# Optimization experiments

Hardware: AMD Instinct MI355X
Metric: run time of the kernel (lower is better)

Reference implementation:

```python
import jax, jax.numpy as jnp
import numpy as np

D_MODEL = 1024
N_HEAD = 16
HEAD_DIM = D_MODEL // N_HEAD


def setup_inputs() -> dict:
    key = jax.random.key(0)
    ks = jax.random.split(key, 9)
    B, S, D = 2, 2048, D_MODEL
    s = 1.0 / np.sqrt(D)
    return {
        "x": jax.random.normal(ks[0], (B, S, D), dtype=jnp.float32),
        "Wq": jax.random.normal(ks[1], (D, D), dtype=jnp.float32) * s,
        "bq": jnp.zeros((D,), dtype=jnp.float32),
        "Wk": jax.random.normal(ks[2], (D, D), dtype=jnp.float32) * s,
        "bk": jnp.zeros((D,), dtype=jnp.float32),
        "Wv": jax.random.normal(ks[3], (D, D), dtype=jnp.float32) * s,
        "bv": jnp.zeros((D,), dtype=jnp.float32),
        "Wo": jax.random.normal(ks[4], (D, D), dtype=jnp.float32) * s,
        "bo": jnp.zeros((D,), dtype=jnp.float32),
    }


def _split_heads(t):
    B, S, D = t.shape
    return t.reshape(B, S, N_HEAD, HEAD_DIM).transpose(0, 2, 1, 3)  # [B,H,S,d]


def reference(x, Wq, bq, Wk, bk, Wv, bv, Wo, bo):
    B, S, D = x.shape
    q = _split_heads(x @ Wq + bq)
    k = _split_heads(x @ Wk + bk)
    v = _split_heads(x @ Wv + bv)
    present = jnp.stack((k, v))  # [2,B,H,S,d]
    # NOTE: module scales by sqrt(d_model), not sqrt(head_dim)
    scores = jnp.einsum("bhqd,bhkd->bhqk", q, k) / jnp.sqrt(jnp.float32(D_MODEL))
    causal = jnp.tril(jnp.ones((S, S), dtype=bool))
    scores = jnp.where(causal, scores, -jnp.inf)
    probs = jax.nn.softmax(scores, axis=-1)
    attn = jnp.einsum("bhqk,bhkd->bhqd", probs, v)
    attn = attn.transpose(0, 2, 1, 3).reshape(B, S, D)
    out = attn @ Wo + bo
    return out, present
```

## Files before the change

### kernel.cpp

```cpp
#include <hip/hip_runtime.h>
#include <hip/hip_bf16.h>

typedef __attribute__((ext_vector_type(8))) short short8;
typedef __attribute__((ext_vector_type(4))) short short4v;
typedef __attribute__((ext_vector_type(4))) float f32x4;

#define S_LEN 2048
#define DM 1024
#define NH 16
#define HD 64

__device__ __forceinline__ short f2b(float f) {
    __hip_bfloat16 h = __float2bfloat16(f);
    return *reinterpret_cast<short*>(&h);
}

__global__ void k_convert_x(const float* __restrict__ x, short* __restrict__ Af) {
    int t = blockIdx.x * 256 + threadIdx.x;
    int s = t >> 7, kc = t & 127;
    const float* xp = x + (size_t)s * DM + kc * 8;
    f32x4 v0 = *reinterpret_cast<const f32x4*>(xp);
    f32x4 v1 = *reinterpret_cast<const f32x4*>(xp + 4);
    short8 o;
    for (int e = 0; e < 4; e++) { o[e] = f2b(v0[e]); o[4 + e] = f2b(v1[e]); }
    int R = s >> 6, m = (s >> 4) & 3, lr = s & 15;
    int kstep = kc >> 3, ks = (kc >> 2) & 1, lg = kc & 3;
    size_t off = ((((size_t)(R * 16 + kstep) * 2 + ks) * 4 + m) * 64 + lg * 16 + lr) * 8;
    *reinterpret_cast<short8*>(Af + off) = o;
}

__global__ void k_transpose_w4(const float* __restrict__ W0, const float* __restrict__ W1,
                               const float* __restrict__ W2, const float* __restrict__ W3,
                               short* __restrict__ T0, short* __restrict__ T1,
                               short* __restrict__ T2, short* __restrict__ T3) {
    __shared__ float tile[32][33];
    const int z = blockIdx.z;
    const float* W = (z == 0) ? W0 : (z == 1) ? W1 : (z == 2) ? W2 : W3;
    short* Wt = (z == 0) ? T0 : (z == 1) ? T1 : (z == 2) ? T2 : T3;
    int tx = threadIdx.x, ty = threadIdx.y;
    int nb = blockIdx.x * 32, kb = blockIdx.y * 32;
    for (int i = 0; i < 4; i++)
        tile[ty + i * 8][tx] = W[(size_t)(kb + ty + i * 8) * DM + nb + tx];
    __syncthreads();
    if (ty < 4) {
        int col = nb + tx;
        int k0 = kb + ty * 8;
        short8 o;
#pragma unroll
        for (int e = 0; e < 8; e++) o[e] = f2b(tile[ty * 8 + e][tx]);
        int C = col >> 6, n = (col >> 4) & 3, lr = col & 15;
        int kstep = k0 >> 6, ksb = (k0 >> 5) & 1, lg = (k0 >> 3) & 3;
        *reinterpret_cast<short8*>(
            &Wt[((((size_t)(C * 16 + kstep) * 2 + ksb) * 4 + n) * 64 + lg * 16 + lr) * 8]) = o;
    }
}

__global__ __launch_bounds__(64) void k_gemm_qkv(
    const short* __restrict__ Af,
    const short* __restrict__ Bq, const short* __restrict__ Bk, const short* __restrict__ Bv,
    const float* __restrict__ bq, const float* __restrict__ bk, const float* __restrict__ bv,
    short* __restrict__ Qb, short* __restrict__ Kfrag, short* __restrict__ Vfrag,
    float* __restrict__ pK, float* __restrict__ pV)
{
    const int bid = blockIdx.x;
    const unsigned orig = (bid & 7) * 384 + (bid >> 3);
    const int R = orig / 48;
    const int rem = orig - R * 48;
    const int z = rem >> 4, C = rem & 15;
    const short* Bf = (z == 0) ? Bq : (z == 1) ? Bk : Bv;
    const float* bias = (z == 0) ? bq : (z == 1) ? bk : bv;
    const int l = threadIdx.x;
    const int lr = l & 15, lg = l >> 4;

    f32x4 acc[4][4];
#pragma unroll
    for (int m = 0; m < 4; m++)
#pragma unroll
        for (int n = 0; n < 4; n++) acc[m][n] = (f32x4)0.0f;

    const short* ap = Af + (size_t)R * 16 * 4096 + l * 8;
    const short* bp = Bf + (size_t)C * 16 * 4096 + l * 8;

#pragma unroll 1
    for (int kstep = 0; kstep < 16; ++kstep) {
        short8 a[2][4], b[2][4];
#pragma unroll
        for (int ks = 0; ks < 2; ks++)
#pragma unroll
            for (int i = 0; i < 4; i++) {
                a[ks][i] = *reinterpret_cast<const short8*>(ap + (ks * 4 + i) * 512);
                b[ks][i] = *reinterpret_cast<const short8*>(bp + (ks * 4 + i) * 512);
            }
        ap += 4096; bp += 4096;
#pragma unroll
        for (int ks = 0; ks < 2; ks++)
#pragma unroll
            for (int m = 0; m < 4; m++)
#pragma unroll
                for (int n = 0; n < 4; n++)
                    acc[m][n] = __builtin_amdgcn_mfma_f32_16x16x32_bf16(a[ks][m], b[ks][n], acc[m][n], 0, 0, 0);
    }

    for (int m = 0; m < 4; m++)
        for (int n = 0; n < 4; n++) {
            int row = R * 64 + m * 16 + lg * 4;
            int col = C * 64 + n * 16 + lr;
            float bv_ = bias[col];
            int b_ = row >> 11, sI0 = row & 2047, hI = col >> 6, dh = col & 63;
            if (z == 0) {
                for (int r = 0; r < 4; r++) {
                    float v = acc[m][n][r] + bv_;
                    Qb[(size_t)(row + r) * DM + col] = f2b(v * 0.0450842200575152f);
                }
            } else if (z == 1) {
                for (int r = 0; r < 4; r++) {
                    float v = acc[m][n][r] + bv_;
                    int sI = sI0 + r;
                    pK[(((size_t)(b_ * NH + hI)) * S_LEN + sI) * HD + dh] = v;
                    int j = sI >> 6, kk = sI & 63;
                    int cg = ((kk >> 4) & 2) | ((kk >> 2) & 1);
                    int lrA = ((kk >> 3) & 3) * 4 + (kk & 3);
                    int lane = lrA + ((dh >> 3) & 3) * 16;
                    int ks = dh >> 5, e = dh & 7;
                    Kfrag[((((size_t)(b_ * NH + hI) * 32 + j) * 2 + ks) * 4 + cg) * 512
                          + lane * 8 + e] = f2b(v);
                }
            } else {
                int j = sI0 >> 6, ks = (sI0 >> 5) & 1;
                int dg = dh >> 4;
                int lane = (dh & 15) + ((sI0 >> 3) & 3) * 16;
                int e0 = sI0 & 7;
                short4v tv;
                for (int r = 0; r < 4; r++) {
                    float v = acc[m][n][r] + bv_;
                    pV[(((size_t)(b_ * NH + hI)) * S_LEN + (sI0 + r)) * HD + dh] = v;
                    tv[r] = f2b(v);
                }
                *reinterpret_cast<short4v*>(
                    &Vfrag[((((size_t)(b_ * NH + hI) * 32 + j) * 2 + ks) * 4 + dg) * 512
                           + lane * 8 + e0]) = tv;
            }
        }
}

__global__ __launch_bounds__(64) void k_gemm_o(
    const short* __restrict__ Af, const short* __restrict__ Bf,
    const float* __restrict__ bo, float* __restrict__ out)
{
    const int bid = blockIdx.x;
    const int orig = (bid & 7) * 128 + (bid >> 3);
    const int R = orig >> 4, C = orig & 15;
    const int l = threadIdx.x;
    const int lr = l & 15, lg = l >> 4;

    f32x4 acc[4][4];
#pragma unroll
    for (int m = 0; m < 4; m++)
#pragma unroll
        for (int n = 0; n < 4; n++) acc[m][n] = (f32x4)0.0f;

    const short* ap = Af + (size_t)R * 16 * 4096 + l * 8;
    const short* bp = Bf + (size_t)C * 16 * 4096 + l * 8;

#pragma unroll 1
    for (int kstep = 0; kstep < 16; ++kstep) {
        short8 a[2][4], b[2][4];
#pragma unroll
        for (int ks = 0; ks < 2; ks++)
#pragma unroll
            for (int i = 0; i < 4; i++) {
                a[ks][i] = *reinterpret_cast<const short8*>(ap + (ks * 4 + i) * 512);
                b[ks][i] = *reinterpret_cast<const short8*>(bp + (ks * 4 + i) * 512);
            }
        ap += 4096; bp += 4096;
#pragma unroll
        for (int ks = 0; ks < 2; ks++)
#pragma unroll
            for (int m = 0; m < 4; m++)
#pragma unroll
                for (int n = 0; n < 4; n++)
                    acc[m][n] = __builtin_amdgcn_mfma_f32_16x16x32_bf16(a[ks][m], b[ks][n], acc[m][n], 0, 0, 0);
    }
    for (int m = 0; m < 4; m++)
        for (int n = 0; n < 4; n++) {
            int row = R * 64 + m * 16 + lg * 4;
            int col = C * 64 + n * 16 + lr;
            float bv_ = bo[col];
            for (int r = 0; r < 4; r++)
                out[(size_t)(row + r) * DM + col] = acc[m][n][r] + bv_;
        }
}

__global__ __launch_bounds__(64) void k_attn(
    const short* __restrict__ Qb, const short* __restrict__ Kfrag,
    const short* __restrict__ Vfrag, short* __restrict__ Afo)
{
    const int bid = blockIdx.x;
    const int orig = (bid & 7) * 256 + (bid >> 3);
    const int bh = orig >> 6;
    const int p = 63 - (orig & 63);
    const int h = bh & 15, b = bh >> 4;
    const int l = threadIdx.x;
    const int lr = l & 15, lg = l >> 4;
    const short* Qp = Qb + (size_t)b * S_LEN * DM + (size_t)h * HD;
    const short* Kbh = Kfrag + (size_t)bh * 32 * 4096;
    const short* Vbh = Vfrag + (size_t)bh * 32 * 4096;

    const int jmax = p >> 1;
    const int sA = 2 * p, sB = 2 * p + 1;
    const int qrowA = sA * 16 + lr, qrowB = sB * 16 + lr;
    short8 qfA0 = *reinterpret_cast<const short8*>(Qp + (size_t)qrowA * DM + lg * 8);
    short8 qfA1 = *reinterpret_cast<const short8*>(Qp + (size_t)qrowA * DM + 32 + lg * 8);
    short8 qfB0 = *reinterpret_cast<const short8*>(Qp + (size_t)qrowB * DM + lg * 8);
    short8 qfB1 = *reinterpret_cast<const short8*>(Qp + (size_t)qrowB * DM + 32 + lg * 8);
    f32x4 oA[4], oB[4];
#pragma unroll
    for (int dg = 0; dg < 4; dg++) { oA[dg] = (f32x4)0.0f; oB[dg] = (f32x4)0.0f; }
    float lrunA = 0.0f, lrunB = 0.0f;

    const short* kp = Kbh + l * 8;
    const short* vp = Vbh + l * 8;
    short8 kc[2][4], vc[2][4];
#pragma unroll
    for (int ks = 0; ks < 2; ks++)
#pragma unroll
        for (int cg = 0; cg < 4; cg++) {
            kc[ks][cg] = *reinterpret_cast<const short8*>(kp + (ks * 4 + cg) * 512);
            vc[ks][cg] = *reinterpret_cast<const short8*>(vp + (ks * 4 + cg) * 512);
        }

    for (int j = 0; j <= jmax; ++j) {
        f32x4 sAcc[4], sBcc[4];
#pragma unroll
        for (int cg = 0; cg < 4; cg++) { sAcc[cg] = (f32x4)0.0f; sBcc[cg] = (f32x4)0.0f; }
#pragma unroll
        for (int ks = 0; ks < 2; ks++) {
            const short8 qfa = ks ? qfA1 : qfA0;
            const short8 qfb = ks ? qfB1 : qfB0;
#pragma unroll
            for (int cg = 0; cg < 4; cg++) {
                sAcc[cg] = __builtin_amdgcn_mfma_f32_16x16x32_bf16(kc[ks][cg], qfa, sAcc[cg], 0, 0, 0);
                sBcc[cg] = __builtin_amdgcn_mfma_f32_16x16x32_bf16(kc[ks][cg], qfb, sBcc[cg], 0, 0, 0);
            }
        }
        if (j < jmax) {
            kp += 4096;
#pragma unroll
            for (int ks = 0; ks < 2; ks++)
#pragma unroll
                for (int cg = 0; cg < 4; cg++)
                    kc[ks][cg] = *reinterpret_cast<const short8*>(kp + (ks * 4 + cg) * 512);
        }
        if (j == jmax) {
#pragma unroll
            for (int cg = 0; cg < 4; cg++)
#pragma unroll
                for (int r = 0; r < 4; r++) {
                    int n = ((cg >> 1) << 5) + (lg << 3) + ((cg & 1) << 2) + r;
                    if (j * 64 + n > qrowA) sAcc[cg][r] = -INFINITY;
                    if (j * 64 + n > qrowB) sBcc[cg][r] = -INFINITY;
                }
        }
        float rsA = 0.0f, rsB = 0.0f;
#pragma unroll
        for (int cg = 0; cg < 4; cg++)
#pragma unroll
            for (int r = 0; r < 4; r++) {
                float pa = __builtin_amdgcn_exp2f(sAcc[cg][r]);
                float pb = __builtin_amdgcn_exp2f(sBcc[cg][r]);
                sAcc[cg][r] = pa; sBcc[cg][r] = pb;
                rsA += pa; rsB += pb;
            }
        lrunA += rsA; lrunB += rsB;
        short8 pfA0, pfA1, pfB0, pfB1;
#pragma unroll
        for (int r = 0; r < 4; r++) {
            pfA0[r] = f2b(sAcc[0][r]); pfA0[4 + r] = f2b(sAcc[1][r]);
            pfA1[r] = f2b(sAcc[2][r]); pfA1[4 + r] = f2b(sAcc[3][r]);
            pfB0[r] = f2b(sBcc[0][r]); pfB0[4 + r] = f2b(sBcc[1][r]);
            pfB1[r] = f2b(sBcc[2][r]); pfB1[4 + r] = f2b(sBcc[3][r]);
        }
#pragma unroll
        for (int ks = 0; ks < 2; ks++) {
            const short8 pfa = ks ? pfA1 : pfA0;
            const short8 pfb = ks ? pfB1 : pfB0;
#pragma unroll
            for (int dg = 0; dg < 4; dg++) {
                oA[dg] = __builtin_amdgcn_mfma_f32_16x16x32_bf16(vc[ks][dg], pfa, oA[dg], 0, 0, 0);
                oB[dg] = __builtin_amdgcn_mfma_f32_16x16x32_bf16(vc[ks][dg], pfb, oB[dg], 0, 0, 0);
            }
        }
        if (j < jmax) {
            vp += 4096;
#pragma unroll
            for (int ks = 0; ks < 2; ks++)
#pragma unroll
                for (int cg = 0; cg < 4; cg++)
                    vc[ks][cg] = *reinterpret_cast<const short8*>(vp + (ks * 4 + cg) * 512);
        }
    }
    lrunA += __shfl_xor(lrunA, 16); lrunA += __shfl_xor(lrunA, 32);
    lrunB += __shfl_xor(lrunB, 16); lrunB += __shfl_xor(lrunB, 32);
    float rinvA = 1.0f / lrunA, rinvB = 1.0f / lrunB;
    const size_t RoA = (size_t)(b * 32 + (sA >> 2));
    const int moA = sA & 3, moB = sB & 3;
#pragma unroll
    for (int dg = 0; dg < 4; dg++) {
        short4v ovA, ovB;
#pragma unroll
        for (int r = 0; r < 4; r++) {
            ovA[r] = f2b(oA[dg][r] * rinvA);
            ovB[r] = f2b(oB[dg][r] * rinvB);
        }
        int lane_o = ((dg & 1) * 2 + (lg >> 1)) * 16 + lr;
        size_t offA = (((RoA * 16 + h) * 2 + (dg >> 1)) * 4 + moA) * 512
                      + (size_t)lane_o * 8 + (lg & 1) * 4;
        size_t offB = (((RoA * 16 + h) * 2 + (dg >> 1)) * 4 + moB) * 512
                      + (size_t)lane_o * 8 + (lg & 1) * 4;
        *reinterpret_cast<short4v*>(Afo + offA) = ovA;
        *reinterpret_cast<short4v*>(Afo + offB) = ovB;
    }
}

extern "C" void kernel_launch(void* const* d_in, const int* in_sizes, int n_in,
                              void* d_out, int out_size, void* d_ws, size_t ws_size,
                              hipStream_t stream) {
    const float* x  = (const float*)d_in[0];
    const float* Wq = (const float*)d_in[1];
    const float* bq = (const float*)d_in[2];
    const float* Wk = (const float*)d_in[3];
    const float* bk = (const float*)d_in[4];
    const float* Wv = (const float*)d_in[5];
    const float* bv = (const float*)d_in[6];
    const float* Wo = (const float*)d_in[7];
    const float* bo = (const float*)d_in[8];

    float* out = (float*)d_out;
    float* presentK = out + (size_t)4194304;
    float* presentV = presentK + (size_t)4194304;

    char* ws = (char*)d_ws;
    short* Af    = (short*)(ws);
    short* Bfq   = (short*)(ws + ((size_t)8  << 20));
    short* Bfk   = (short*)(ws + ((size_t)10 << 20));
    short* Bfv   = (short*)(ws + ((size_t)12 << 20));
    short* Bfo   = (short*)(ws + ((size_t)14 << 20));
    short* Qb    = (short*)(ws + ((size_t)16 << 20));
    short* Kfrag = (short*)(ws + ((size_t)24 << 20));
    short* Vfrag = (short*)(ws + ((size_t)32 << 20));
    short* Afo   = (short*)(ws + ((size_t)40 << 20));

    k_convert_x<<<dim3(2048), dim3(256), 0, stream>>>(x, Af);
    k_transpose_w4<<<dim3(32, 32, 4), dim3(32, 8), 0, stream>>>(
        Wq, Wk, Wv, Wo, Bfq, Bfk, Bfv, Bfo);
    k_gemm_qkv<<<dim3(3072), dim3(64), 0, stream>>>(
        Af, Bfq, Bfk, Bfv, bq, bk, bv, Qb, Kfrag, Vfrag, presentK, presentV);
    k_attn<<<dim3(2048), dim3(64), 0, stream>>>(Qb, Kfrag, Vfrag, Afo);
    k_gemm_o<<<dim3(1024), dim3(64), 0, stream>>>(Afo, Bfo, bo, out);
}
```

Before: 116.6 us.

## Share QKV weight tiles across four waves via double-buffered LDS

The QKV GEMM block grows from one wave to four, each wave computing a different 64-row tile against the same 64-column weight tile. The weight tile is staged into a double-buffered LDS region with direct global-to-LDS loads, prefetching the next k-step while the current one is computed. This is meant to cut redundant global/L2 traffic for the weight operand by four. In exchange it adds a block barrier per k-step and changes the grid remapping to 768 blocks.

```diff
diff --git a/kernel.cpp b/kernel.cpp
--- a/kernel.cpp
+++ b/kernel.cpp
@@ -13,6 +13,12 @@
 __device__ __forceinline__ short f2b(float f) {
     __hip_bfloat16 h = __float2bfloat16(f);
     return *reinterpret_cast<short*>(&h);
+}
+
+__device__ __forceinline__ void gload_lds16(const void* g, void* l) {
+    __builtin_amdgcn_global_load_lds(
+        (const __attribute__((address_space(1))) unsigned int*)g,
+        (__attribute__((address_space(3))) unsigned int*)l, 16, 0, 0);
 }
 
 __global__ void k_convert_x(const float* __restrict__ x, short* __restrict__ Af) {
@@ -55,21 +61,23 @@
     }
 }
 
-__global__ __launch_bounds__(64) void k_gemm_qkv(
+__global__ __launch_bounds__(256) void k_gemm_qkv(
     const short* __restrict__ Af,
     const short* __restrict__ Bq, const short* __restrict__ Bk, const short* __restrict__ Bv,
     const float* __restrict__ bq, const float* __restrict__ bk, const float* __restrict__ bv,
     short* __restrict__ Qb, short* __restrict__ Kfrag, short* __restrict__ Vfrag,
     float* __restrict__ pK, float* __restrict__ pV)
 {
+    __shared__ alignas(16) short Bs[2][4096];
     const int bid = blockIdx.x;
-    const unsigned orig = (bid & 7) * 384 + (bid >> 3);
-    const int R = orig / 48;
-    const int rem = orig - R * 48;
+    const int orig = (bid & 7) * 96 + (bid >> 3);
+    const int Rg = orig / 48;
+    const int rem = orig - Rg * 48;
     const int z = rem >> 4, C = rem & 15;
     const short* Bf = (z == 0) ? Bq : (z == 1) ? Bk : Bv;
     const float* bias = (z == 0) ? bq : (z == 1) ? bk : bv;
-    const int l = threadIdx.x;
+    const int w = threadIdx.x >> 6, l = threadIdx.x & 63;
+    const int R = Rg * 4 + w;
     const int lr = l & 15, lg = l >> 4;
 
     f32x4 acc[4][4];
@@ -79,19 +87,35 @@
         for (int n = 0; n < 4; n++) acc[m][n] = (f32x4)0.0f;
 
     const short* ap = Af + (size_t)R * 16 * 4096 + l * 8;
-    const short* bp = Bf + (size_t)C * 16 * 4096 + l * 8;
+    const short* bp = Bf + (size_t)C * 16 * 4096;
+
+#pragma unroll
+    for (int p = 0; p < 2; p++) {
+        int idx = p * 256 + threadIdx.x;
+        gload_lds16(bp + idx * 8, &Bs[0][0] + idx * 8);
+    }
 
 #pragma unroll 1
     for (int kstep = 0; kstep < 16; ++kstep) {
+        const int cur = kstep & 1;
+        __syncthreads();
+        if (kstep < 15) {
+            const short* bn = bp + (kstep + 1) * 4096;
+#pragma unroll
+            for (int p = 0; p < 2; p++) {
+                int idx = p * 256 + threadIdx.x;
+                gload_lds16(bn + idx * 8, &Bs[cur ^ 1][0] + idx * 8);
+            }
+        }
         short8 a[2][4], b[2][4];
 #pragma unroll
         for (int ks = 0; ks < 2; ks++)
 #pragma unroll
             for (int i = 0; i < 4; i++) {
                 a[ks][i] = *reinterpret_cast<const short8*>(ap + (ks * 4 + i) * 512);
-                b[ks][i] = *reinterpret_cast<const short8*>(bp + (ks * 4 + i) * 512);
-            }
-        ap += 4096; bp += 4096;
+                b[ks][i] = *reinterpret_cast<const short8*>(&Bs[cur][(ks * 4 + i) * 512 + l * 8]);
+            }
+        ap += 4096;
 #pragma unroll
         for (int ks = 0; ks < 2; ks++)
 #pragma unroll
@@ -353,7 +377,7 @@
     k_convert_x<<<dim3(2048), dim3(256), 0, stream>>>(x, Af);
     k_transpose_w4<<<dim3(32, 32, 4), dim3(32, 8), 0, stream>>>(
         Wq, Wk, Wv, Wo, Bfq, Bfk, Bfv, Bfo);
-    k_gemm_qkv<<<dim3(3072), dim3(64), 0, stream>>>(
+    k_gemm_qkv<<<dim3(768), dim3(256), 0, stream>>>(
         Af, Bfq, Bfk, Bfv, bq, bk, bv, Qb, Kfrag, Vfrag, presentK, presentV);
     k_attn<<<dim3(2048), dim3(64), 0, stream>>>(Qb, Kfrag, Vfrag, Afo);
     k_gemm_o<<<dim3(1024), dim3(64), 0, stream>>>(Afo, Bfo, bo, out);
```

After: 131.7 us. +13.0%, slower.
